# Performance work log

Hardware: AMD Instinct MI355X
Metric: run time of the kernel (lower is better)

Reference implementation:

```python
import jax, jax.numpy as jnp
import numpy as np

K_NN = 9  # kernel_size: neighbors per node (includes self, dist 0)


def knn_edges(feat):
    """feat: (B, C, N). Replicates DenseDilatedKnnGraph (dilation=1):
    L2-normalize over channels, dense pairwise sq-distance, top-k nearest."""
    nrm = jnp.sqrt(jnp.sum(feat * feat, axis=1, keepdims=True))
    xn = feat / jnp.maximum(nrm, 1e-12)            # F.normalize(dim=1)
    xt = jnp.swapaxes(xn, 1, 2)                    # (B, N, C)
    sq = jnp.sum(xt * xt, axis=-1)                 # (B, N)
    dist = sq[:, :, None] + sq[:, None, :] - 2.0 * jnp.einsum('bnc,bmc->bnm', xt, xt)
    _, nn_idx = jax.lax.top_k(-dist, K_NN)         # (B, N, k)
    center = jnp.broadcast_to(jnp.arange(nn_idx.shape[1], dtype=nn_idx.dtype)[None, :, None], nn_idx.shape)
    return nn_idx, center                          # (x_j sources, x_i targets)


def reference(x, W0, W1, bias):
    B, C, H, W = x.shape
    N = H * W
    NB = B * N
    feat = x.reshape(B, C, N)
    # KNN graph is built on detached features in the torch source
    x_j, x_i = knn_edges(jax.lax.stop_gradient(feat))
    E = B * N * K_NN
    # faithful to source: torch.linspace(0, B, steps=E, dtype=int64) batch offsets
    count = jnp.linspace(0.0, float(B), E).astype(jnp.int32)
    src = x_j.reshape(-1).astype(jnp.int32) + count * N
    dst = x_i.reshape(-1).astype(jnp.int32) + count * N
    valid = (src < NB) & (dst < NB)                # drop the out-of-range tail edge
    # flat_nodes: (B, C, H, W) -> (B*H*W, C), node id = b*HW + pixel
    nodes = jnp.swapaxes(feat, 1, 2).reshape(NB, C)
    # ChebConv K=2, sym norm, lambda_max=2: Tx0 = x, Tx1 = -(D^-1/2 A D^-1/2) x
    w = valid.astype(nodes.dtype)
    deg = jax.ops.segment_sum(w, src, num_segments=NB)
    dinv = jnp.where(deg > 0, jax.lax.rsqrt(jnp.maximum(deg, 1.0)), 0.0)
    norm = -(dinv[src] * w * dinv[dst])            # scaled-Laplacian edge weights
    msg = norm[:, None] * nodes[src]               # (E, C) gather + weight
    Tx1 = jax.ops.segment_sum(msg, dst, num_segments=NB)
    return nodes @ W0 + Tx1 @ W1 + bias


def setup_inputs() -> dict:
    key = jax.random.key(0)
    k1, k2, k3, k4 = jax.random.split(key, 4)
    B, C, H, W = 8, 48, 64, 64
    Cout = 48
    s = 1.0 / np.sqrt(C)
    return {
        'x': jax.random.normal(k1, (B, C, H, W), dtype=jnp.float32),
        'W0': jax.random.normal(k2, (C, Cout), dtype=jnp.float32) * s,
        'W1': jax.random.normal(k3, (C, Cout), dtype=jnp.float32) * s,
        'bias': jax.random.normal(k4, (Cout,), dtype=jnp.float32) * 0.01,
    }
```

## Files before the change

### kernel.cpp

```cpp
#include <hip/hip_runtime.h>

#define BATCH 8
#define CH    48
#define NPTS  4096
#define NBN   (BATCH*NPTS)
#define KNN   9
#define NCAND 12

typedef unsigned short u16;
typedef unsigned int   u32;
typedef unsigned long long u64;
typedef __bf16 bf16x8 __attribute__((ext_vector_type(8)));
typedef float  f32x4  __attribute__((ext_vector_type(4)));

__device__ __forceinline__ float bf2f(u16 v) { return __uint_as_float(((u32)v) << 16); }
__device__ __forceinline__ u16 f2bf(float f) {
  u32 u = __float_as_uint(f);
  u = (u + 0x7fffu + ((u >> 16) & 1u)) >> 16;
  return (u16)u;
}

#define MED3U(d, a, b, c) \
  asm("v_med3_u32 %0, %1, %2, %3" : "=v"(d) : "v"(a), "v"(b), "v"(c))
#define INS12(p0,p1,p2,p3,p4,p5,p6,p7,p8,p9,p10,p11,x) do { \
  MED3U(p11,p10,p11,x); MED3U(p10,p9,p10,x); MED3U(p9,p8,p9,x);  \
  MED3U(p8, p7, p8, x); MED3U(p7, p6,p7, x); MED3U(p6,p5,p6,x);  \
  MED3U(p5, p4, p5, x); MED3U(p4, p3,p4, x); MED3U(p3,p2,p3,x);  \
  MED3U(p2, p1, p2, x); MED3U(p1, p0,p1, x); p0 = min(p0, x);    \
} while (0)

__device__ __forceinline__ void stage_q(const u16* g, u16* l) {
  __builtin_amdgcn_global_load_lds(
      (const __attribute__((address_space(1))) void*)g,
      (__attribute__((address_space(3))) void*)l, 16, 0, 0);
}

__global__ __launch_bounds__(64)
void k_prep(const float* __restrict__ x, float* __restrict__ xraw,
            float* __restrict__ xn, float* __restrict__ csq,
            u16* __restrict__ Abuf, u16* __restrict__ Bbuf,
            int* __restrict__ deg) {
  __shared__ __align__(16) float xrawS[64 * 48];
  __shared__ __align__(16) float xnS[64 * 48];
  __shared__ __align__(16) u16   AS[64 * 128];
  __shared__ __align__(16) u16   BS[64 * 128];
  int tid = threadIdx.x;
  int node0 = blockIdx.x * 64;
  int node = node0 + tid;
  deg[node] = 0;
  int b = node >> 12, n = node & (NPTS - 1);
  const float* xb = x + (size_t)b * CH * NPTS;
  float f[CH];
#pragma unroll
  for (int c = 0; c < CH; ++c) f[c] = xb[(size_t)c * NPTS + n];
  float a0 = 0, a1 = 0, a2 = 0, a3 = 0;
#pragma unroll
  for (int k = 0; k < CH; k += 4) {
    a0 += f[k] * f[k]; a1 += f[k+1] * f[k+1];
    a2 += f[k+2] * f[k+2]; a3 += f[k+3] * f[k+3];
  }
  float nrm = fmaxf(sqrtf((a0 + a1) + (a2 + a3)), 1e-12f);
  float rn = 1.0f / nrm;
  a0 = a1 = a2 = a3 = 0;
#pragma unroll
  for (int k = 0; k < CH; k += 4) {
    float v0 = f[k]*rn, v1 = f[k+1]*rn, v2 = f[k+2]*rn, v3 = f[k+3]*rn;
    a0 += v0*v0; a1 += v1*v1; a2 += v2*v2; a3 += v3*v3;
  }
  float csqv = (a0 + a1) + (a2 + a3);
  csq[node] = csqv;
  float4* ro = (float4*)(xrawS + tid * 48);
  float4* no = (float4*)(xnS   + tid * 48);
#pragma unroll
  for (int i = 0; i < CH / 4; ++i) {
    ro[i] = make_float4(f[4*i], f[4*i+1], f[4*i+2], f[4*i+3]);
    no[i] = make_float4(f[4*i]*rn, f[4*i+1]*rn, f[4*i+2]*rn, f[4*i+3]*rn);
  }
  uint4* Bo = (uint4*)(BS + tid * 128);
  u16* Ag = AS + (tid >> 4) * 2048 + (tid & 15) * 8;
#pragma unroll
  for (int g = 0; g < 6; ++g) {
    u32 bhw[4], blw[4], ahw[4], alw[4];
#pragma unroll
    for (int j = 0; j < 4; ++j) {
      int k = g * 8 + j * 2;
      float v0 = f[k] * rn, v1 = f[k+1] * rn;
      u16 h0 = f2bf(v0), h1 = f2bf(v1);
      u16 l0 = f2bf(v0 - bf2f(h0)), l1 = f2bf(v1 - bf2f(h1));
      bhw[j] = (u32)h0 | ((u32)h1 << 16);
      blw[j] = (u32)l0 | ((u32)l1 << 16);
      float w0 = -2.0f * v0, w1 = -2.0f * v1;
      u16 g0 = f2bf(w0), g1 = f2bf(w1);
      u16 m0 = f2bf(w0 - bf2f(g0)), m1 = f2bf(w1 - bf2f(g1));
      ahw[j] = (u32)g0 | ((u32)g1 << 16);
      alw[j] = (u32)m0 | ((u32)m1 << 16);
    }
    Bo[g]     = make_uint4(bhw[0], bhw[1], bhw[2], bhw[3]);
    Bo[8 + g] = make_uint4(blw[0], blw[1], blw[2], blw[3]);
    int v = g >> 2, q = g & 3;
    *(uint4*)(Ag + v * 512 + q * 128)        = make_uint4(ahw[0], ahw[1], ahw[2], ahw[3]);
    *(uint4*)(Ag + 1024 + v * 512 + q * 128) = make_uint4(alw[0], alw[1], alw[2], alw[3]);
  }
  {
    u16 h = f2bf(csqv); u16 l = f2bf(csqv - bf2f(h));
    Bo[6]  = make_uint4(0x3F80u, 0, 0, 0);
    Bo[14] = make_uint4(0, 0, 0, 0);
    *(uint4*)(Ag + 512 + 2 * 128)        = make_uint4((u32)h, 0, 0, 0);
    *(uint4*)(Ag + 1024 + 512 + 2 * 128) = make_uint4((u32)l, 0, 0, 0);
  }
  {
    uint4 z = make_uint4(0, 0, 0, 0);
    Bo[7] = z; Bo[15] = z;
    *(uint4*)(Ag + 512 + 3 * 128)        = z;
    *(uint4*)(Ag + 1024 + 512 + 3 * 128) = z;
  }
  __syncthreads();
  {
    float4* xrg = (float4*)(xraw + (size_t)node0 * CH);
    float4* xng = (float4*)(xn   + (size_t)node0 * CH);
    const float4* xrs = (const float4*)xrawS;
    const float4* xns = (const float4*)xnS;
    for (int i = tid; i < 64 * 48 / 4; i += 64) { xrg[i] = xrs[i]; xng[i] = xns[i]; }
    uint4* Agl = (uint4*)(Abuf + (size_t)(node0 >> 4) * 2048);
    const uint4* As4 = (const uint4*)AS;
    for (int i = tid; i < 64 * 128 / 8; i += 64) Agl[i] = As4[i];
    uint4* Bgl = (uint4*)(Bbuf + (size_t)node0 * 128);
    const uint4* Bs4 = (const uint4*)BS;
    for (int i = tid; i < 64 * 128 / 8; i += 64) Bgl[i] = Bs4[i];
  }
}

__global__ __launch_bounds__(256, 6)
void k_knn_m(const u16* __restrict__ Abuf, const u16* __restrict__ Bbuf,
             u32* __restrict__ candu) {
  __shared__ __align__(16) u16 As[4][2048];
  int tid = threadIdx.x;
  int lane = tid & 63;
  int wv = tid >> 6;
  int quad = lane >> 4, m16 = lane & 15;
  int panel = blockIdx.x * 4 + wv;
  int row = panel * 16 + m16;
  int b4096 = row & ~(NPTS - 1);
  int quarter = blockIdx.y;
  int ct0 = quarter * 64;

  const __bf16* Bb = (const __bf16*)Bbuf + (size_t)row * 128;
  bf16x8 bh0 = *(const bf16x8*)(Bb + quad * 8);
  bf16x8 bh1 = *(const bf16x8*)(Bb + 32 + quad * 8);
  bf16x8 bl0 = *(const bf16x8*)(Bb + 64 + quad * 8);
  bf16x8 bl1 = *(const bf16x8*)(Bb + 96 + quad * 8);

  const u16* gs = Abuf + ((size_t)(b4096 >> 4) + ct0) * 2048
                  + wv * 512 + lane * 8;

  u32 s0=~0u,s1=~0u,s2=~0u,s3=~0u,s4=~0u,s5=~0u,
      s6=~0u,s7=~0u,s8=~0u,s9=~0u,s10=~0u,s11=~0u;

  const f32x4 C25 = {2.5f, 2.5f, 2.5f, 2.5f};

#define BARRIER() __builtin_amdgcn_s_barrier()
#define VMC(N) asm volatile("s_waitcnt vmcnt(" #N ")" ::: "memory")
#define LDA(SL, A0,A1,A2,A3) do {                                           \
    const u16* _p = &As[SL][lane * 8];                                      \
    A0 = *(const bf16x8*)(_p);                                              \
    A1 = *(const bf16x8*)(_p + 512);                                        \
    A2 = *(const bf16x8*)(_p + 1024);                                       \
    A3 = *(const bf16x8*)(_p + 1536);                                       \
  } while (0)
#define MFMA6(ACC, A0,A1,A2,A3) do {                                        \
    ACC = __builtin_amdgcn_mfma_f32_16x16x32_bf16(A0, bh0, C25, 0, 0, 0);   \
    ACC = __builtin_amdgcn_mfma_f32_16x16x32_bf16(A1, bh1, ACC, 0, 0, 0);   \
    ACC = __builtin_amdgcn_mfma_f32_16x16x32_bf16(A0, bl0, ACC, 0, 0, 0);   \
    ACC = __builtin_amdgcn_mfma_f32_16x16x32_bf16(A1, bl1, ACC, 0, 0, 0);   \
    ACC = __builtin_amdgcn_mfma_f32_16x16x32_bf16(A2, bh0, ACC, 0, 0, 0);   \
    ACC = __builtin_amdgcn_mfma_f32_16x16x32_bf16(A3, bh1, ACC, 0, 0, 0);   \
  } while (0)
#define FILTER(ACC, CT) do {                                                \
    u32 _colb = ((u32)(CT) << 4) | ((u32)quad << 2);                        \
    _Pragma("unroll")                                                       \
    for (int _r = 0; _r < 4; ++_r) {                                        \
      u32 _u = __float_as_uint((ACC)[_r]);                                  \
      u32 _x = (_u & 0xFFFFF000u) | (_colb | (u32)_r);                      \
      INS12(s0,s1,s2,s3,s4,s5,s6,s7,s8,s9,s10,s11, _x);                     \
    }                                                                       \
  } while (0)

  f32x4 accA, accB;
  bf16x8 a0, a1, a2, a3;

  stage_q(gs,                    &As[0][wv * 512]);
  stage_q(gs + (size_t)1 * 2048, &As[1][wv * 512]);
  stage_q(gs + (size_t)2 * 2048, &As[2][wv * 512]);
  VMC(2);
  BARRIER();

  stage_q(gs + (size_t)3 * 2048, &As[3][wv * 512]);
  LDA(0, a0, a1, a2, a3);
  MFMA6(accA, a0, a1, a2, a3);
  VMC(2);
  BARRIER();

  for (int p = 0; p < 30; ++p) {
    int tA = 2 * p + 1;
    stage_q(gs + (size_t)(tA + 3) * 2048, &As[(tA + 3) & 3][wv * 512]);
    LDA(tA & 3, a0, a1, a2, a3);
    MFMA6(accB, a0, a1, a2, a3);
    FILTER(accA, ct0 + tA - 1);
    VMC(2);
    BARRIER();

    int tB = tA + 1;
    stage_q(gs + (size_t)(tB + 3) * 2048, &As[(tB + 3) & 3][wv * 512]);
    LDA(tB & 3, a0, a1, a2, a3);
    MFMA6(accA, a0, a1, a2, a3);
    FILTER(accB, ct0 + tB - 1);
    VMC(2);
    BARRIER();
  }
  LDA(61 & 3, a0, a1, a2, a3);
  MFMA6(accB, a0, a1, a2, a3);
  FILTER(accA, ct0 + 60);
  VMC(1);
  BARRIER();

  LDA(62 & 3, a0, a1, a2, a3);
  MFMA6(accA, a0, a1, a2, a3);
  FILTER(accB, ct0 + 61);
  VMC(0);
  BARRIER();

  LDA(63 & 3, a0, a1, a2, a3);
  MFMA6(accB, a0, a1, a2, a3);
  FILTER(accA, ct0 + 62);
  FILTER(accB, ct0 + 63);
#undef BARRIER
#undef VMC
#undef LDA
#undef MFMA6
#undef FILTER

#define CE(a,b) { u32 _lo = min(a, b); b = max(a, b); a = _lo; }
  {
    u32 p0 = __shfl_xor(s0, 16),  p1 = __shfl_xor(s1, 16);
    u32 p2 = __shfl_xor(s2, 16),  p3 = __shfl_xor(s3, 16);
    u32 p4 = __shfl_xor(s4, 16),  p5 = __shfl_xor(s5, 16);
    u32 p6 = __shfl_xor(s6, 16),  p7 = __shfl_xor(s7, 16);
    u32 p8 = __shfl_xor(s8, 16),  p9 = __shfl_xor(s9, 16);
    u32 p10 = __shfl_xor(s10, 16), p11 = __shfl_xor(s11, 16);
    s0 = min(s0, p11); s1 = min(s1, p10); s2 = min(s2, p9);
    s3 = min(s3, p8);  s4 = min(s4, p7);  s5 = min(s5, p6);
    s6 = min(s6, p5);  s7 = min(s7, p4);  s8 = min(s8, p3);
    s9 = min(s9, p2);  s10 = min(s10, p1); s11 = min(s11, p0);
    CE(s0, s8)  CE(s1, s9)  CE(s2, s10) CE(s3, s11)
    CE(s0, s4)  CE(s1, s5)  CE(s2, s6)  CE(s3, s7)
    CE(s0, s2)  CE(s1, s3)  CE(s4, s6)  CE(s5, s7)
    CE(s8, s10) CE(s9, s11)
    CE(s0, s1)  CE(s2, s3)  CE(s4, s5)  CE(s6, s7)
    CE(s8, s9)  CE(s10, s11)
  }
  {
    u32 p0 = __shfl_xor(s0, 32),  p1 = __shfl_xor(s1, 32);
    u32 p2 = __shfl_xor(s2, 32),  p3 = __shfl_xor(s3, 32);
    u32 p4 = __shfl_xor(s4, 32),  p5 = __shfl_xor(s5, 32);
    u32 p6 = __shfl_xor(s6, 32),  p7 = __shfl_xor(s7, 32);
    u32 p8 = __shfl_xor(s8, 32),  p9 = __shfl_xor(s9, 32);
    u32 p10 = __shfl_xor(s10, 32), p11 = __shfl_xor(s11, 32);
    s0 = min(s0, p11); s1 = min(s1, p10); s2 = min(s2, p9);
    s3 = min(s3, p8);  s4 = min(s4, p7);  s5 = min(s5, p6);
    s6 = min(s6, p5);  s7 = min(s7, p4);  s8 = min(s8, p3);
    s9 = min(s9, p2);  s10 = min(s10, p1); s11 = min(s11, p0);
  }
#undef CE
  if (quad == 0) {
    u32* o = candu + ((size_t)row * 4 + quarter) * NCAND;
    o[0]=s0; o[1]=s1; o[2]=s2; o[3]=s3; o[4]=s4; o[5]=s5;
    o[6]=s6; o[7]=s7; o[8]=s8; o[9]=s9; o[10]=s10; o[11]=s11;
  }
}

#define RWS 32
__global__ __launch_bounds__(256)
void k_rr(const u32* __restrict__ candu, const float* __restrict__ xn,
          const float* __restrict__ csq, u16* __restrict__ nn,
          int* __restrict__ deg) {
  __shared__ int cs[RWS][12];
  __shared__ __align__(16) float xnS[RWS][52];
  __shared__ float csqS[RWS];
  __shared__ float dS[RWS][12];
  __shared__ int   iS[RWS][12];
  int tid = threadIdx.x, bi = blockIdx.x;
  int row0 = (bi & 7) * NPTS + (bi >> 3) * RWS;
  int b4096 = row0 & ~(NPTS - 1);
  for (int i = tid; i < RWS * 12; i += 256) {
    int ln = i / 12, f4 = i % 12;
    *(float4*)&xnS[ln][f4 * 4] =
        *(const float4*)(xn + (size_t)(row0 + ln) * CH + f4 * 4);
  }
  if (tid < RWS) csqS[tid] = csq[row0 + tid];
  if (tid < RWS) {
    const uint4* src = (const uint4*)(candu + (size_t)(row0 + tid) * 48);
    u32 g0=~0u,g1=~0u,g2=~0u,g3=~0u,g4=~0u,g5=~0u,
        g6=~0u,g7=~0u,g8=~0u,g9=~0u,g10=~0u,g11=~0u;
#pragma unroll
    for (int s = 0; s < 12; ++s) {
      uint4 v = src[s];
      INS12(g0,g1,g2,g3,g4,g5,g6,g7,g8,g9,g10,g11, v.x);
      INS12(g0,g1,g2,g3,g4,g5,g6,g7,g8,g9,g10,g11, v.y);
      INS12(g0,g1,g2,g3,g4,g5,g6,g7,g8,g9,g10,g11, v.z);
      INS12(g0,g1,g2,g3,g4,g5,g6,g7,g8,g9,g10,g11, v.w);
    }
    cs[tid][0]=(int)(g0&0xFFFu);  cs[tid][1]=(int)(g1&0xFFFu);
    cs[tid][2]=(int)(g2&0xFFFu);  cs[tid][3]=(int)(g3&0xFFFu);
    cs[tid][4]=(int)(g4&0xFFFu);  cs[tid][5]=(int)(g5&0xFFFu);
    cs[tid][6]=(int)(g6&0xFFFu);  cs[tid][7]=(int)(g7&0xFFFu);
    cs[tid][8]=(int)(g8&0xFFFu);  cs[tid][9]=(int)(g9&0xFFFu);
    cs[tid][10]=(int)(g10&0xFFFu); cs[tid][11]=(int)(g11&0xFFFu);
  }
  __syncthreads();
  for (int task = tid; task < RWS * 12; task += 256) {
    int r = task / 12, j = task % 12;
    int c = cs[r][j] & (NPTS - 1);
    const float4* cp = (const float4*)(xn + (size_t)(b4096 + c) * CH);
    const float* rf = &xnS[r][0];
    float a0 = 0, a1 = 0, a2 = 0, a3 = 0;
#pragma unroll
    for (int i = 0; i < CH / 4; ++i) {
      float4 v = cp[i];
      a0 += rf[4*i]   * v.x; a1 += rf[4*i+1] * v.y;
      a2 += rf[4*i+2] * v.z; a3 += rf[4*i+3] * v.w;
    }
    float dist = (csqS[r] + csq[b4096 + c]) - 2.0f * ((a0 + a1) + (a2 + a3));
    dS[r][j] = dist; iS[r][j] = c;
  }
  __syncthreads();
  if (tid < RWS) {
    int lr = tid;
    int row = row0 + lr;
    float gd[KNN]; int gi[KNN];
#pragma unroll
    for (int j = 0; j < KNN; ++j) { gd[j] = 3.4e38f; gi[j] = 0x7fffffff; }
    for (int s = 0; s < NCAND; ++s) {
      float dc = dS[lr][s]; int ic = iS[lr][s];
      if (dc < gd[KNN - 1] || (dc == gd[KNN - 1] && ic < gi[KNN - 1])) {
        gd[KNN - 1] = dc; gi[KNN - 1] = ic;
#pragma unroll
        for (int k2 = KNN - 1; k2 > 0; --k2) {
          bool sw = (gd[k2] < gd[k2 - 1]) ||
                    (gd[k2] == gd[k2 - 1] && gi[k2] < gi[k2 - 1]);
          if (sw) {
            float td = gd[k2]; gd[k2] = gd[k2 - 1]; gd[k2 - 1] = td;
            int ti = gi[k2]; gi[k2] = gi[k2 - 1]; gi[k2 - 1] = ti;
          }
        }
      }
    }
    u16* o = nn + (size_t)row * KNN;
    int jmax = (row == NBN - 1) ? (KNN - 1) : KNN;
#pragma unroll
    for (int j = 0; j < KNN; ++j) o[j] = (u16)(gi[j] & (NPTS - 1));
    for (int j = 0; j < jmax; ++j)
      atomicAdd(&deg[b4096 + (gi[j] & (NPTS - 1))], 1);
  }
}

#define ONB 32
#define LPAD 52
__global__ __launch_bounds__(256)
void k_out_f(const float* __restrict__ xraw, const u16* __restrict__ nn,
             const int* __restrict__ deg,
             const float* __restrict__ W0, const float* __restrict__ W1,
             const float* __restrict__ bias, float* __restrict__ out) {
  __shared__ float w0[CH * CH], w1[CH * CH], bs[CH];
  __shared__ __align__(16) float fS[ONB * LPAD];
  __shared__ __align__(16) float txS[ONB * LPAD];
  __shared__ float dinvS[ONB];
  int tid = threadIdx.x;
  int bi = blockIdx.x;
  int n0 = (bi & 7) * NPTS + (bi >> 3) * ONB;
  int b12 = n0 & ~(NPTS - 1);
  for (int i = tid; i < CH * CH; i += 256) { w0[i] = W0[i]; w1[i] = W1[i]; }
  if (tid < CH) bs[tid] = bias[tid];
  for (int i = tid; i < ONB * 12; i += 256) {
    int ln = i / 12, f4 = i % 12;
    *(float4*)(fS + ln * LPAD + f4 * 4) =
        *(const float4*)(xraw + (size_t)(n0 + ln) * CH + f4 * 4);
  }
  if (tid < ONB) {
    int dg = deg[n0 + tid];
    dinvS[tid] = (dg > 0) ? (1.0f / sqrtf((float)dg)) : 0.0f;
  }
  __syncthreads();

  int ln = tid >> 3, p = tid & 7;
  int node = n0 + ln;
  float dn = dinvS[ln];
  const u16* nrow = nn + (size_t)node * KNN;
  bool full = (node != NBN - 1);
  float tx[6];
#pragma unroll
  for (int i = 0; i < 6; ++i) tx[i] = 0.f;
#pragma unroll
  for (int j = 0; j < KNN; ++j) {
    if (j < KNN - 1 || full) {
      int s = nrow[j] & (NPTS - 1);
      int dgs = deg[b12 + s];
      float ds = (dgs > 0) ? (1.0f / sqrtf((float)dgs)) : 0.0f;
      float w = -(ds * dn);
      const float2* pr = (const float2*)(xraw + (size_t)(b12 + s) * CH + p * 6);
#pragma unroll
      for (int q3 = 0; q3 < 3; ++q3) {
        float2 v = pr[q3];
        tx[q3*2]   += w * v.x; tx[q3*2+1] += w * v.y;
      }
    }
  }
#pragma unroll
  for (int q3 = 0; q3 < 3; ++q3)
    *(float2*)(txS + ln * LPAD + p * 6 + q3 * 2) =
        make_float2(tx[q3*2], tx[q3*2+1]);
  __syncthreads();

  float acc[6];
#pragma unroll
  for (int i = 0; i < 6; ++i) acc[i] = bs[p * 6 + i];
  const float* fr = fS + ln * LPAD;
  const float* tr = txS + ln * LPAD;
#pragma unroll
  for (int c = 0; c < CH; ++c) {
    float fc = fr[c];
    const float* wr = w0 + c * CH + p * 6;
#pragma unroll
    for (int i = 0; i < 6; ++i) acc[i] += fc * wr[i];
  }
#pragma unroll
  for (int c = 0; c < CH; ++c) {
    float tc = tr[c];
    const float* wr = w1 + c * CH + p * 6;
#pragma unroll
    for (int i = 0; i < 6; ++i) acc[i] += tc * wr[i];
  }
  float* op = out + (size_t)node * CH + p * 6;
#pragma unroll
  for (int q3 = 0; q3 < 3; ++q3)
    *(float2*)(op + q3 * 2) = make_float2(acc[q3*2], acc[q3*2+1]);
}

__global__ __launch_bounds__(256)
void k_zero(int* __restrict__ deg) { deg[blockIdx.x * 256 + threadIdx.x] = 0; }

__global__ __launch_bounds__(256)
void k_hist(const u16* __restrict__ nn, int* __restrict__ deg) {
  int node = blockIdx.x * 256 + threadIdx.x;
  int b12 = node & ~(NPTS - 1);
  int jmax = (node == NBN - 1) ? (KNN - 1) : KNN;
  for (int j = 0; j < jmax; ++j)
    atomicAdd(&deg[b12 + (nn[(size_t)node * KNN + j] & (NPTS - 1))], 1);
}

__global__ __launch_bounds__(256)
void k_dinv(const int* __restrict__ deg, float* __restrict__ dinv) {
  int i = blockIdx.x * 256 + threadIdx.x;
  int dg = deg[i];
  dinv[i] = (dg > 0) ? (1.0f / sqrtf((float)dg)) : 0.0f;
}

#define NQ    4
#define QCOLS (NPTS/NQ)
#define TCOLS 32
#define NTILES (QCOLS/TCOLS)
#define RPB   64

__global__ __launch_bounds__(256)
void k_knn_nb(const float* __restrict__ x, u16* __restrict__ nn) {
  __shared__ __align__(16) float tile[NQ * TCOLS * CH];
  __shared__ float nrmS[NQ * TCOLS];
  __shared__ float csq[NQ * TCOLS];
  int tid = threadIdx.x;
  int r0 = blockIdx.x * RPB;
  int b  = r0 >> 12;
  int q  = tid >> 6;
  int lr = tid & 63;
  int n  = (r0 + lr) & (NPTS - 1);
  const float* xb = x + (size_t)b * CH * NPTS;
  float rf[CH];
#pragma unroll
  for (int c = 0; c < CH; ++c) rf[c] = xb[(size_t)c * NPTS + n];
  float sqn;
  {
    float a0 = 0, a1 = 0, a2 = 0, a3 = 0;
#pragma unroll
    for (int k = 0; k < CH; k += 4) {
      a0 += rf[k] * rf[k]; a1 += rf[k+1] * rf[k+1];
      a2 += rf[k+2] * rf[k+2]; a3 += rf[k+3] * rf[k+3];
    }
    float nrm = fmaxf(sqrtf((a0 + a1) + (a2 + a3)), 1e-12f);
#pragma unroll
    for (int c = 0; c < CH; ++c) rf[c] = rf[c] / nrm;
    a0 = a1 = a2 = a3 = 0;
#pragma unroll
    for (int k = 0; k < CH; k += 4) {
      a0 += rf[k] * rf[k]; a1 += rf[k+1] * rf[k+1];
      a2 += rf[k+2] * rf[k+2]; a3 += rf[k+3] * rf[k+3];
    }
    sqn = (a0 + a1) + (a2 + a3);
  }
  float d[KNN]; int id[KNN];
#pragma unroll
  for (int j = 0; j < KNN; ++j) { d[j] = 3.4e38f; id[j] = 0x7fffffff; }
  for (int t = 0; t < NTILES; ++t) {
    __syncthreads();
#pragma unroll
    for (int qq = 0; qq < NQ; ++qq) {
      int colbase = qq * QCOLS + t * TCOLS;
      float* dst = tile + qq * TCOLS * CH;
#pragma unroll
      for (int it = 0; it < 6; ++it) {
        int i = it * 256 + tid;
        int c = i >> 5, p = i & 31;
        dst[p * CH + c] = xb[(size_t)c * NPTS + colbase + p];
      }
    }
    __syncthreads();
    if (tid < NQ * TCOLS) {
      const float* cp = tile + tid * CH;
      float a0 = 0, a1 = 0, a2 = 0, a3 = 0;
#pragma unroll
      for (int k = 0; k < CH; k += 4) {
        float4 v = *(const float4*)(cp + k);
        a0 += v.x * v.x; a1 += v.y * v.y; a2 += v.z * v.z; a3 += v.w * v.w;
      }
      nrmS[tid] = fmaxf(sqrtf((a0 + a1) + (a2 + a3)), 1e-12f);
    }
    __syncthreads();
    for (int i = tid; i < NQ * TCOLS * CH; i += 256)
      tile[i] = tile[i] / nrmS[i / CH];
    __syncthreads();
    if (tid < NQ * TCOLS) {
      const float* cp = tile + tid * CH;
      float a0 = 0, a1 = 0, a2 = 0, a3 = 0;
#pragma unroll
      for (int k = 0; k < CH; k += 4) {
        float4 v = *(const float4*)(cp + k);
        a0 += v.x * v.x; a1 += v.y * v.y; a2 += v.z * v.z; a3 += v.w * v.w;
      }
      csq[tid] = (a0 + a1) + (a2 + a3);
    }
    __syncthreads();
    int cbase = q * QCOLS + t * TCOLS;
    const float* tq = tile + q * TCOLS * CH;
    for (int cc = 0; cc < TCOLS; ++cc) {
      const float* cp = tq + cc * CH;
      float a0 = 0, a1 = 0, a2 = 0, a3 = 0;
#pragma unroll
      for (int k = 0; k < CH; k += 4) {
        float4 v = *(const float4*)(cp + k);
        a0 += rf[k] * v.x; a1 += rf[k+1] * v.y;
        a2 += rf[k+2] * v.z; a3 += rf[k+3] * v.w;
      }
      float dist = (sqn + csq[q * TCOLS + cc]) - 2.0f * ((a0 + a1) + (a2 + a3));
      if (dist < d[KNN - 1]) {
        d[KNN - 1] = dist; id[KNN - 1] = cbase + cc;
#pragma unroll
        for (int k2 = KNN - 1; k2 > 0; --k2) {
          if (d[k2] < d[k2 - 1]) {
            float td = d[k2]; d[k2] = d[k2 - 1]; d[k2 - 1] = td;
            int ti = id[k2]; id[k2] = id[k2 - 1]; id[k2 - 1] = ti;
          }
        }
      }
    }
  }
  __syncthreads();
  float* md = tile;
  int*   mi = (int*)(tile + 256 * KNN);
#pragma unroll
  for (int j = 0; j < KNN; ++j) { md[tid * KNN + j] = d[j]; mi[tid * KNN + j] = id[j]; }
  __syncthreads();
  if (tid < RPB) {
    float fd[KNN]; int fi[KNN];
#pragma unroll
    for (int j = 0; j < KNN; ++j) { fd[j] = 3.4e38f; fi[j] = 0x7fffffff; }
    for (int qq = 0; qq < NQ; ++qq) {
      int s = qq * RPB + tid;
      for (int j = 0; j < KNN; ++j) {
        float dc = md[s * KNN + j]; int ic = mi[s * KNN + j];
        if (dc < fd[KNN - 1]) {
          fd[KNN - 1] = dc; fi[KNN - 1] = ic;
#pragma unroll
          for (int k2 = KNN - 1; k2 > 0; --k2) {
            if (fd[k2] < fd[k2 - 1]) {
              float td = fd[k2]; fd[k2] = fd[k2 - 1]; fd[k2 - 1] = td;
              int ti = fi[k2]; fi[k2] = fi[k2 - 1]; fi[k2 - 1] = ti;
            }
          }
        }
      }
    }
    u16* o = nn + (size_t)(r0 + tid) * KNN;
#pragma unroll
    for (int j = 0; j < KNN; ++j) o[j] = (u16)(fi[j] & (NPTS - 1));
  }
}

__global__ __launch_bounds__(256)
void k_out_nb(const float* __restrict__ x, const u16* __restrict__ nn,
              const float* __restrict__ dinv,
              const float* __restrict__ W0, const float* __restrict__ W1,
              const float* __restrict__ bias, float* __restrict__ out) {
  __shared__ float w0[CH * CH], w1[CH * CH], bs[CH];
  for (int i = threadIdx.x; i < CH * CH; i += 256) { w0[i] = W0[i]; w1[i] = W1[i]; }
  if (threadIdx.x < CH) bs[threadIdx.x] = bias[threadIdx.x];
  __syncthreads();
  int node = blockIdx.x * 256 + threadIdx.x;
  int b = node >> 12, n = node & (NPTS - 1);
  const float* xb = x + (size_t)b * CH * NPTS;
  float f[CH], acc[CH], tx[CH];
#pragma unroll
  for (int c = 0; c < CH; ++c) f[c] = xb[(size_t)c * NPTS + n];
#pragma unroll
  for (int o = 0; o < CH; ++o) acc[o] = bs[o];
#pragma unroll
  for (int c = 0; c < CH; ++c) {
    float fc = f[c];
    const float* wr = w0 + c * CH;
#pragma unroll
    for (int o = 0; o < CH; ++o) acc[o] += fc * wr[o];
  }
#pragma unroll
  for (int c = 0; c < CH; ++c) tx[c] = 0.f;
  float dn = dinv[node];
  int jmax = (node == NBN - 1) ? (KNN - 1) : KNN;
  for (int j = 0; j < jmax; ++j) {
    int s = nn[(size_t)node * KNN + j] & (NPTS - 1);
    float w = -(dinv[(b << 12) + s] * dn);
#pragma unroll
    for (int c = 0; c < CH; ++c) tx[c] += w * xb[(size_t)c * NPTS + s];
  }
#pragma unroll
  for (int c = 0; c < CH; ++c) {
    float tc = tx[c];
    const float* wr = w1 + c * CH;
#pragma unroll
    for (int o = 0; o < CH; ++o) acc[o] += tc * wr[o];
  }
  float4* op = (float4*)(out + (size_t)node * CH);
#pragma unroll
  for (int i = 0; i < CH / 4; ++i)
    op[i] = make_float4(acc[4*i], acc[4*i+1], acc[4*i+2], acc[4*i+3]);
}

extern "C" void kernel_launch(void* const* d_in, const int* in_sizes, int n_in,
                              void* d_out, int out_size, void* d_ws, size_t ws_size,
                              hipStream_t stream) {
  const float* x    = (const float*)d_in[0];
  const float* W0   = (const float*)d_in[1];
  const float* W1   = (const float*)d_in[2];
  const float* bias = (const float*)d_in[3];
  float* out = (float*)d_out;
  char* w = (char*)d_ws;

  const size_t SZ_XN   = (size_t)NBN * CH * 4;
  const size_t SZ_XRAW = (size_t)NBN * CH * 4;
  const size_t SZ_CSQ  = (size_t)NBN * 4;
  const size_t SZ_NN   = (size_t)NBN * KNN * 2;
  const size_t SZ_DEG  = (size_t)NBN * 4;
  const size_t SZ_AB   = (size_t)NBN * 128 * 2;
  const size_t SZ_CU   = (size_t)NBN * 4 * NCAND * 4;
  const size_t needF = SZ_XN + SZ_XRAW + SZ_CSQ + SZ_NN + SZ_DEG
                     + 2 * SZ_AB + SZ_CU;

  if (ws_size >= needF) {
    size_t off = 0;
    float* xn   = (float*)(w + off); off += SZ_XN;
    float* xraw = (float*)(w + off); off += SZ_XRAW;
    float* csq  = (float*)(w + off); off += SZ_CSQ;
    u16*   nn   = (u16*)  (w + off); off += SZ_NN;
    int*   deg  = (int*)  (w + off); off += SZ_DEG;
    u16*   Abuf = (u16*)  (w + off); off += SZ_AB;
    u16*   Bbuf = (u16*)  (w + off); off += SZ_AB;
    u32*   candu= (u32*)  (w + off);
    k_prep    <<<NBN / 64, 64, 0, stream>>>(x, xraw, xn, csq, Abuf, Bbuf, deg);
    k_knn_m   <<<dim3(NBN / 64, 4), 256, 0, stream>>>(Abuf, Bbuf, candu);
    k_rr      <<<NBN / RWS, 256, 0, stream>>>(candu, xn, csq, nn, deg);
    k_out_f   <<<NBN / ONB, 256, 0, stream>>>(xraw, nn, deg, W0, W1, bias, out);
  } else {
    u16*   nn   = (u16*)w;
    int*   deg  = (int*)(w + SZ_NN);
    float* dinv = (float*)(w + SZ_NN + SZ_DEG);
    k_knn_nb <<<NBN / RPB, 256, 0, stream>>>(x, nn);
    k_zero   <<<NBN / 256, 256, 0, stream>>>(deg);
    k_hist   <<<NBN / 256, 256, 0, stream>>>(nn, deg);
    k_dinv   <<<NBN / 256, 256, 0, stream>>>(deg, dinv);
    k_out_nb <<<NBN / 256, 256, 0, stream>>>(x, nn, dinv, W0, W1, bias, out);
  }
}
```

Measured before the change: 192.2 us.

## Drop Bbuf staging, build B operands in-kernel, and parallelize candidate merge

The prep kernel no longer writes the bf16 hi/lo B-operand buffer. The KNN matmul kernel now builds those operands directly from the normalized fp32 features, which removes an 8 MB write and read through global memory. The 4-way candidate merge in k_rr is spread over 4 lanes per row using shuffles and bitonic-style cleanup instead of serial insertion by one thread. The wave-level merge in k_knn_m also swaps to a different cleanup network applied after both shuffle stages, which adds some ALU work per lane.

```diff
diff --git a/kernel.cpp b/kernel.cpp
--- a/kernel.cpp
+++ b/kernel.cpp
@@ -29,6 +29,17 @@
   MED3U(p2, p1, p2, x); MED3U(p1, p0,p1, x); p0 = min(p0, x);    \
 } while (0)
 
+#define CEx(a,b) { u32 _lo = min(a, b); b = max(a, b); a = _lo; }
+#define SORT3(a,b,c) { CEx(a,b) CEx(b,c) CEx(a,b) }
+#define CLEAN12V(s0,s1,s2,s3,s4,s5,s6,s7,s8,s9,s10,s11) do { \
+  CEx(s0, s6)  CEx(s1, s7)  CEx(s2, s8)                      \
+  CEx(s3, s9)  CEx(s4, s10) CEx(s5, s11)                     \
+  CEx(s0, s3)  CEx(s1, s4)  CEx(s2, s5)                      \
+  CEx(s6, s9)  CEx(s7, s10) CEx(s8, s11)                     \
+  SORT3(s0, s1, s2)   SORT3(s3, s4, s5)                      \
+  SORT3(s6, s7, s8)   SORT3(s9, s10, s11)                    \
+} while (0)
+
 __device__ __forceinline__ void stage_q(const u16* g, u16* l) {
   __builtin_amdgcn_global_load_lds(
       (const __attribute__((address_space(1))) void*)g,
@@ -38,12 +49,10 @@
 __global__ __launch_bounds__(64)
 void k_prep(const float* __restrict__ x, float* __restrict__ xraw,
             float* __restrict__ xn, float* __restrict__ csq,
-            u16* __restrict__ Abuf, u16* __restrict__ Bbuf,
-            int* __restrict__ deg) {
+            u16* __restrict__ Abuf, int* __restrict__ deg) {
   __shared__ __align__(16) float xrawS[64 * 48];
   __shared__ __align__(16) float xnS[64 * 48];
   __shared__ __align__(16) u16   AS[64 * 128];
-  __shared__ __align__(16) u16   BS[64 * 128];
   int tid = threadIdx.x;
   int node0 = blockIdx.x * 64;
   int node = node0 + tid;
@@ -76,41 +85,31 @@
     ro[i] = make_float4(f[4*i], f[4*i+1], f[4*i+2], f[4*i+3]);
     no[i] = make_float4(f[4*i]*rn, f[4*i+1]*rn, f[4*i+2]*rn, f[4*i+3]*rn);
   }
-  uint4* Bo = (uint4*)(BS + tid * 128);
   u16* Ag = AS + (tid >> 4) * 2048 + (tid & 15) * 8;
 #pragma unroll
   for (int g = 0; g < 6; ++g) {
-    u32 bhw[4], blw[4], ahw[4], alw[4];
+    u32 ahw[4], alw[4];
 #pragma unroll
     for (int j = 0; j < 4; ++j) {
       int k = g * 8 + j * 2;
       float v0 = f[k] * rn, v1 = f[k+1] * rn;
-      u16 h0 = f2bf(v0), h1 = f2bf(v1);
-      u16 l0 = f2bf(v0 - bf2f(h0)), l1 = f2bf(v1 - bf2f(h1));
-      bhw[j] = (u32)h0 | ((u32)h1 << 16);
-      blw[j] = (u32)l0 | ((u32)l1 << 16);
       float w0 = -2.0f * v0, w1 = -2.0f * v1;
       u16 g0 = f2bf(w0), g1 = f2bf(w1);
       u16 m0 = f2bf(w0 - bf2f(g0)), m1 = f2bf(w1 - bf2f(g1));
       ahw[j] = (u32)g0 | ((u32)g1 << 16);
       alw[j] = (u32)m0 | ((u32)m1 << 16);
     }
-    Bo[g]     = make_uint4(bhw[0], bhw[1], bhw[2], bhw[3]);
-    Bo[8 + g] = make_uint4(blw[0], blw[1], blw[2], blw[3]);
     int v = g >> 2, q = g & 3;
     *(uint4*)(Ag + v * 512 + q * 128)        = make_uint4(ahw[0], ahw[1], ahw[2], ahw[3]);
     *(uint4*)(Ag + 1024 + v * 512 + q * 128) = make_uint4(alw[0], alw[1], alw[2], alw[3]);
   }
   {
     u16 h = f2bf(csqv); u16 l = f2bf(csqv - bf2f(h));
-    Bo[6]  = make_uint4(0x3F80u, 0, 0, 0);
-    Bo[14] = make_uint4(0, 0, 0, 0);
     *(uint4*)(Ag + 512 + 2 * 128)        = make_uint4((u32)h, 0, 0, 0);
     *(uint4*)(Ag + 1024 + 512 + 2 * 128) = make_uint4((u32)l, 0, 0, 0);
   }
   {
     uint4 z = make_uint4(0, 0, 0, 0);
-    Bo[7] = z; Bo[15] = z;
     *(uint4*)(Ag + 512 + 3 * 128)        = z;
     *(uint4*)(Ag + 1024 + 512 + 3 * 128) = z;
   }
@@ -124,14 +123,11 @@
     uint4* Agl = (uint4*)(Abuf + (size_t)(node0 >> 4) * 2048);
     const uint4* As4 = (const uint4*)AS;
     for (int i = tid; i < 64 * 128 / 8; i += 64) Agl[i] = As4[i];
-    uint4* Bgl = (uint4*)(Bbuf + (size_t)node0 * 128);
-    const uint4* Bs4 = (const uint4*)BS;
-    for (int i = tid; i < 64 * 128 / 8; i += 64) Bgl[i] = Bs4[i];
   }
 }
 
 __global__ __launch_bounds__(256, 6)
-void k_knn_m(const u16* __restrict__ Abuf, const u16* __restrict__ Bbuf,
+void k_knn_m(const u16* __restrict__ Abuf, const float* __restrict__ xn,
              u32* __restrict__ candu) {
   __shared__ __align__(16) u16 As[4][2048];
   int tid = threadIdx.x;
@@ -144,11 +140,25 @@
   int quarter = blockIdx.y;
   int ct0 = quarter * 64;
 
-  const __bf16* Bb = (const __bf16*)Bbuf + (size_t)row * 128;
-  bf16x8 bh0 = *(const bf16x8*)(Bb + quad * 8);
-  bf16x8 bh1 = *(const bf16x8*)(Bb + 32 + quad * 8);
-  bf16x8 bl0 = *(const bf16x8*)(Bb + 64 + quad * 8);
-  bf16x8 bl1 = *(const bf16x8*)(Bb + 96 + quad * 8);
+  bf16x8 bh0, bh1, bl0, bl1;
+  {
+    const float* xr = xn + (size_t)row * CH;
+    union { u16 u[8]; bf16x8 v; } H0, L0, H1, L1;
+#pragma unroll
+    for (int j = 0; j < 8; ++j) {
+      float v = xr[quad * 8 + j];
+      u16 h = f2bf(v);
+      H0.u[j] = h; L0.u[j] = f2bf(v - bf2f(h));
+    }
+#pragma unroll
+    for (int j = 0; j < 8; ++j) {
+      int k = 32 + quad * 8 + j;
+      float v = (k < 48) ? xr[k] : ((k == 48) ? 1.0f : 0.0f);
+      u16 h = f2bf(v);
+      H1.u[j] = h; L1.u[j] = f2bf(v - bf2f(h));
+    }
+    bh0 = H0.v; bl0 = L0.v; bh1 = H1.v; bl1 = L1.v;
+  }
 
   const u16* gs = Abuf + ((size_t)(b4096 >> 4) + ct0) * 2048
                   + wv * 512 + lane * 8;
@@ -239,7 +249,6 @@
 #undef MFMA6
 #undef FILTER
 
-#define CE(a,b) { u32 _lo = min(a, b); b = max(a, b); a = _lo; }
   {
     u32 p0 = __shfl_xor(s0, 16),  p1 = __shfl_xor(s1, 16);
     u32 p2 = __shfl_xor(s2, 16),  p3 = __shfl_xor(s3, 16);
@@ -251,12 +260,7 @@
     s3 = min(s3, p8);  s4 = min(s4, p7);  s5 = min(s5, p6);
     s6 = min(s6, p5);  s7 = min(s7, p4);  s8 = min(s8, p3);
     s9 = min(s9, p2);  s10 = min(s10, p1); s11 = min(s11, p0);
-    CE(s0, s8)  CE(s1, s9)  CE(s2, s10) CE(s3, s11)
-    CE(s0, s4)  CE(s1, s5)  CE(s2, s6)  CE(s3, s7)
-    CE(s0, s2)  CE(s1, s3)  CE(s4, s6)  CE(s5, s7)
-    CE(s8, s10) CE(s9, s11)
-    CE(s0, s1)  CE(s2, s3)  CE(s4, s5)  CE(s6, s7)
-    CE(s8, s9)  CE(s10, s11)
+    CLEAN12V(s0,s1,s2,s3,s4,s5,s6,s7,s8,s9,s10,s11);
   }
   {
     u32 p0 = __shfl_xor(s0, 32),  p1 = __shfl_xor(s1, 32);
@@ -269,8 +273,8 @@
     s3 = min(s3, p8);  s4 = min(s4, p7);  s5 = min(s5, p6);
     s6 = min(s6, p5);  s7 = min(s7, p4);  s8 = min(s8, p3);
     s9 = min(s9, p2);  s10 = min(s10, p1); s11 = min(s11, p0);
-  }
-#undef CE
+    CLEAN12V(s0,s1,s2,s3,s4,s5,s6,s7,s8,s9,s10,s11);
+  }
   if (quad == 0) {
     u32* o = candu + ((size_t)row * 4 + quarter) * NCAND;
     o[0]=s0; o[1]=s1; o[2]=s2; o[3]=s3; o[4]=s4; o[5]=s5;
@@ -297,24 +301,45 @@
         *(const float4*)(xn + (size_t)(row0 + ln) * CH + f4 * 4);
   }
   if (tid < RWS) csqS[tid] = csq[row0 + tid];
-  if (tid < RWS) {
-    const uint4* src = (const uint4*)(candu + (size_t)(row0 + tid) * 48);
-    u32 g0=~0u,g1=~0u,g2=~0u,g3=~0u,g4=~0u,g5=~0u,
-        g6=~0u,g7=~0u,g8=~0u,g9=~0u,g10=~0u,g11=~0u;
-#pragma unroll
-    for (int s = 0; s < 12; ++s) {
-      uint4 v = src[s];
-      INS12(g0,g1,g2,g3,g4,g5,g6,g7,g8,g9,g10,g11, v.x);
-      INS12(g0,g1,g2,g3,g4,g5,g6,g7,g8,g9,g10,g11, v.y);
-      INS12(g0,g1,g2,g3,g4,g5,g6,g7,g8,g9,g10,g11, v.z);
-      INS12(g0,g1,g2,g3,g4,g5,g6,g7,g8,g9,g10,g11, v.w);
-    }
-    cs[tid][0]=(int)(g0&0xFFFu);  cs[tid][1]=(int)(g1&0xFFFu);
-    cs[tid][2]=(int)(g2&0xFFFu);  cs[tid][3]=(int)(g3&0xFFFu);
-    cs[tid][4]=(int)(g4&0xFFFu);  cs[tid][5]=(int)(g5&0xFFFu);
-    cs[tid][6]=(int)(g6&0xFFFu);  cs[tid][7]=(int)(g7&0xFFFu);
-    cs[tid][8]=(int)(g8&0xFFFu);  cs[tid][9]=(int)(g9&0xFFFu);
-    cs[tid][10]=(int)(g10&0xFFFu); cs[tid][11]=(int)(g11&0xFFFu);
+  if (tid < RWS * 4) {
+    int r = tid >> 2, q = tid & 3;
+    const uint4* src = (const uint4*)(candu + ((size_t)(row0 + r) * 4 + q) * NCAND);
+    uint4 va = src[0], vb = src[1], vc = src[2];
+    u32 m0=va.x, m1=va.y, m2=va.z, m3=va.w, m4=vb.x, m5=vb.y,
+        m6=vb.z, m7=vb.w, m8=vc.x, m9=vc.y, m10=vc.z, m11=vc.w;
+    {
+      u32 p0 = __shfl_xor(m0, 1),  p1 = __shfl_xor(m1, 1);
+      u32 p2 = __shfl_xor(m2, 1),  p3 = __shfl_xor(m3, 1);
+      u32 p4 = __shfl_xor(m4, 1),  p5 = __shfl_xor(m5, 1);
+      u32 p6 = __shfl_xor(m6, 1),  p7 = __shfl_xor(m7, 1);
+      u32 p8 = __shfl_xor(m8, 1),  p9 = __shfl_xor(m9, 1);
+      u32 p10 = __shfl_xor(m10, 1), p11 = __shfl_xor(m11, 1);
+      m0 = min(m0, p11); m1 = min(m1, p10); m2 = min(m2, p9);
+      m3 = min(m3, p8);  m4 = min(m4, p7);  m5 = min(m5, p6);
+      m6 = min(m6, p5);  m7 = min(m7, p4);  m8 = min(m8, p3);
+      m9 = min(m9, p2);  m10 = min(m10, p1); m11 = min(m11, p0);
+      CLEAN12V(m0,m1,m2,m3,m4,m5,m6,m7,m8,m9,m10,m11);
+    }
+    {
+      u32 p0 = __shfl_xor(m0, 2),  p1 = __shfl_xor(m1, 2);
+      u32 p2 = __shfl_xor(m2, 2),  p3 = __shfl_xor(m3, 2);
+      u32 p4 = __shfl_xor(m4, 2),  p5 = __shfl_xor(m5, 2);
+      u32 p6 = __shfl_xor(m6, 2),  p7 = __shfl_xor(m7, 2);
+      u32 p8 = __shfl_xor(m8, 2),  p9 = __shfl_xor(m9, 2);
+      u32 p10 = __shfl_xor(m10, 2), p11 = __shfl_xor(m11, 2);
+      m0 = min(m0, p11); m1 = min(m1, p10); m2 = min(m2, p9);
+      m3 = min(m3, p8);  m4 = min(m4, p7);  m5 = min(m5, p6);
+      m6 = min(m6, p5);  m7 = min(m7, p4);  m8 = min(m8, p3);
+      m9 = min(m9, p2);  m10 = min(m10, p1); m11 = min(m11, p0);
+    }
+    if (q == 0) {
+      cs[r][0]=(int)(m0&0xFFFu);  cs[r][1]=(int)(m1&0xFFFu);
+      cs[r][2]=(int)(m2&0xFFFu);  cs[r][3]=(int)(m3&0xFFFu);
+      cs[r][4]=(int)(m4&0xFFFu);  cs[r][5]=(int)(m5&0xFFFu);
+      cs[r][6]=(int)(m6&0xFFFu);  cs[r][7]=(int)(m7&0xFFFu);
+      cs[r][8]=(int)(m8&0xFFFu);  cs[r][9]=(int)(m9&0xFFFu);
+      cs[r][10]=(int)(m10&0xFFFu); cs[r][11]=(int)(m11&0xFFFu);
+    }
   }
   __syncthreads();
   for (int task = tid; task < RWS * 12; task += 256) {
@@ -667,7 +692,7 @@
   const size_t SZ_AB   = (size_t)NBN * 128 * 2;
   const size_t SZ_CU   = (size_t)NBN * 4 * NCAND * 4;
   const size_t needF = SZ_XN + SZ_XRAW + SZ_CSQ + SZ_NN + SZ_DEG
-                     + 2 * SZ_AB + SZ_CU;
+                     + SZ_AB + SZ_CU;
 
   if (ws_size >= needF) {
     size_t off = 0;
@@ -677,10 +702,9 @@
     u16*   nn   = (u16*)  (w + off); off += SZ_NN;
     int*   deg  = (int*)  (w + off); off += SZ_DEG;
     u16*   Abuf = (u16*)  (w + off); off += SZ_AB;
-    u16*   Bbuf = (u16*)  (w + off); off += SZ_AB;
     u32*   candu= (u32*)  (w + off);
-    k_prep    <<<NBN / 64, 64, 0, stream>>>(x, xraw, xn, csq, Abuf, Bbuf, deg);
-    k_knn_m   <<<dim3(NBN / 64, 4), 256, 0, stream>>>(Abuf, Bbuf, candu);
+    k_prep    <<<NBN / 64, 64, 0, stream>>>(x, xraw, xn, csq, Abuf, deg);
+    k_knn_m   <<<dim3(NBN / 64, 4), 256, 0, stream>>>(Abuf, xn, candu);
     k_rr      <<<NBN / RWS, 256, 0, stream>>>(candu, xn, csq, nn, deg);
     k_out_f   <<<NBN / ONB, 256, 0, stream>>>(xraw, nn, deg, W0, W1, bias, out);
   } else {
```

Result: slower. 196.1 us (+2.0%).
